# Kernel tuning notes

Hardware: AMD Instinct MI355X
Metric: run time of the kernel (lower is better)

## Reference

```python
import jax, jax.numpy as jnp
import numpy as np

B, C, H, W = 16, 512, 64, 64
K = 32


def setup_inputs() -> dict:
    key = jax.random.key(0)
    k1, k2, k3 = jax.random.split(key, 3)
    std = 1.0 / (64 * C) ** 0.5
    x = jax.random.normal(k1, (B, C, H, W), dtype=jnp.float32)
    codewords = jax.random.uniform(k2, (K, C), dtype=jnp.float32, minval=-std, maxval=std)
    scale = jax.random.uniform(k3, (K,), dtype=jnp.float32, minval=-1.0, maxval=0.0)
    return {"x": x, "codewords": codewords, "scale": scale}


def reference(x, codewords, scale):
    b, c, h, w = x.shape
    # (b, n, c) with n = h*w spatial positions
    xf = x.reshape(b, c, h * w).transpose(0, 2, 1)
    x2 = jnp.sum(xf * xf, axis=-1)                       # (b, n)
    c2 = jnp.sum(codewords * codewords, axis=-1)          # (k,)
    xc = jnp.einsum('bnc,kc->bnk', xf, codewords)         # (b, n, k)
    logits = scale[None, None, :] * (x2[:, :, None] - 2.0 * xc + c2[None, None, :])
    A = jax.nn.softmax(logits, axis=2)                    # (b, n, k)
    # sum_n A[b,n,k] * (x[b,n,c] - codewords[k,c])
    encoded = jnp.einsum('bnk,bnc->bkc', A, xf) - jnp.einsum('bnk,kc->bkc', A, codewords)
    return encoded
```

## Files before the change

kernel.cpp:

```cpp
#include <hip/hip_runtime.h>
#include <hip/hip_bf16.h>
#include <math.h>

#define BB 16
#define CC 512
#define NN 4096
#define KK 32

typedef __attribute__((ext_vector_type(8))) short short8;
typedef __attribute__((ext_vector_type(4))) float float4v;

static __device__ __forceinline__ unsigned short f2bf(float f) {
  unsigned u = __float_as_uint(f);
  u += 0x7FFF + ((u >> 16) & 1);
  return (unsigned short)(u >> 16);
}
static __device__ __forceinline__ float bf2f(unsigned short s) {
  return __uint_as_float(((unsigned)s) << 16);
}


__global__ __launch_bounds__(256) void prep_kernel(
    const float* __restrict__ cw, unsigned short* __restrict__ cwt2,
    float* __restrict__ c2, float* __restrict__ out) {
  int gid = blockIdx.x * 256 + threadIdx.x;
  float4v z = {0.f, 0.f, 0.f, 0.f};
  float4v* o4 = (float4v*)out;
#pragma unroll
  for (int j = 0; j < 4; ++j) o4[gid + j * 16384] = z;
  {
    int c = gid >> 5, k = gid & 31;
    cwt2[gid] = f2bf(cw[k * CC + c]);
  }
  __shared__ float c2p[KK][8];
  if (blockIdx.x == 0) {
    int k = threadIdx.x >> 3, j = threadIdx.x & 7;
    const float* row = cw + k * CC + j * 64;
    float s = 0.f;
    for (int i = 0; i < 64; ++i) s = fmaf(row[i], row[i], s);
    c2p[k][j] = s;
    __syncthreads();
    if (threadIdx.x < KK) {
      float t = 0.f;
      for (int j2 = 0; j2 < 8; ++j2) t += c2p[threadIdx.x][j2];
      c2[threadIdx.x] = t;
    }
  }
}

__global__ __launch_bounds__(256) void logits_kernel(
    const float* __restrict__ x, const unsigned short* __restrict__ cwt2,
    const float* __restrict__ c2g, const float* __restrict__ scale,
    unsigned short* __restrict__ A) {
  const int b = blockIdx.x >> 4;
  const int n0 = (blockIdx.x & 15) << 8;
  const int t = threadIdx.x;
  const int kq = t & 3;
  const int pq = t >> 2;

  __shared__ float Xl[2][8][258];
  __shared__ unsigned short Sm[256][34];

  const float* xb = x + (size_t)b * CC * NN + n0;

  float sc[8], cc2[8];
#pragma unroll
  for (int i = 0; i < 8; ++i) {
    sc[i] = scale[8 * kq + i];
    cc2[i] = c2g[8 * kq + i];
  }

  float acc[8][4];
#pragma unroll
  for (int i = 0; i < 8; ++i)
#pragma unroll
    for (int p = 0; p < 4; ++p) acc[i][p] = 0.f;
  float x2[4] = {0.f, 0.f, 0.f, 0.f};

  float4v pf[2];
#pragma unroll
  for (int j = 0; j < 2; ++j) {
    int f = t + 256 * j;
    int row = f >> 6, c4 = f & 63;
    pf[j] = *(const float4v*)(xb + (size_t)row * NN + c4 * 4);
  }
#pragma unroll
  for (int j = 0; j < 2; ++j) {
    int f = t + 256 * j;
    int row = f >> 6, c4 = f & 63;
    *(float4v*)&Xl[0][row][c4 * 4] = pf[j];
  }
  __syncthreads();

  int cur = 0;
  for (int ch = 0; ch < 64; ++ch) {
    const int cbase = ch * 8;
    if (ch < 63) {
#pragma unroll
      for (int j = 0; j < 2; ++j) {
        int f = t + 256 * j;
        int row = f >> 6, c4 = f & 63;
        pf[j] = *(const float4v*)(xb + (size_t)(cbase + 8 + row) * NN + c4 * 4);
      }
    }
#pragma unroll
    for (int c = 0; c < 8; ++c) {
      float4v xv = *(const float4v*)&Xl[cur][c][4 * pq];
      short8 cwv = *(const short8*)(cwt2 + (size_t)(cbase + c) * 32 + 8 * kq);
      float cf[8];
#pragma unroll
      for (int i = 0; i < 8; ++i) cf[i] = bf2f(((unsigned short*)&cwv)[i]);
      x2[0] = fmaf(xv.x, xv.x, x2[0]);
      x2[1] = fmaf(xv.y, xv.y, x2[1]);
      x2[2] = fmaf(xv.z, xv.z, x2[2]);
      x2[3] = fmaf(xv.w, xv.w, x2[3]);
#pragma unroll
      for (int i = 0; i < 8; ++i) {
        acc[i][0] = fmaf(cf[i], xv.x, acc[i][0]);
        acc[i][1] = fmaf(cf[i], xv.y, acc[i][1]);
        acc[i][2] = fmaf(cf[i], xv.z, acc[i][2]);
        acc[i][3] = fmaf(cf[i], xv.w, acc[i][3]);
      }
    }
    if (ch < 63) {
      int nxt = cur ^ 1;
#pragma unroll
      for (int j = 0; j < 2; ++j) {
        int f = t + 256 * j;
        int row = f >> 6, c4 = f & 63;
        *(float4v*)&Xl[nxt][row][c4 * 4] = pf[j];
      }
      __syncthreads();
      cur = nxt;
    }
  }

#pragma unroll
  for (int p = 0; p < 4; ++p) {
    float l[8];
    float m = -INFINITY;
#pragma unroll
    for (int i = 0; i < 8; ++i) {
      float lg = sc[i] * (x2[p] - 2.f * acc[i][p] + cc2[i]);
      l[i] = lg;
      m = fmaxf(m, lg);
    }
    m = fmaxf(m, __shfl_xor(m, 1));
    m = fmaxf(m, __shfl_xor(m, 2));
    float s = 0.f;
#pragma unroll
    for (int i = 0; i < 8; ++i) {
      float e = __expf(l[i] - m);
      l[i] = e;
      s += e;
    }
    s += __shfl_xor(s, 1);
    s += __shfl_xor(s, 2);
    float inv = 1.0f / s;
    const int pos = 4 * pq + p;
#pragma unroll
    for (int i = 0; i < 8; ++i) Sm[pos][8 * kq + i] = f2bf(l[i] * inv);
  }
  __syncthreads();

#pragma unroll
  for (int k = 0; k < KK; ++k) {
    A[((size_t)(b * KK + k)) * NN + n0 + t] = Sm[t][k];
  }
}

__global__ __launch_bounds__(256) void agg_kernel(
    const float* __restrict__ x, const unsigned short* __restrict__ A,
    float* __restrict__ out) {
  const int b = blockIdx.x >> 4;
  const int n0 = (blockIdx.x & 15) << 8;
  const int t = threadIdx.x;
  const int w = t >> 6;
  const int l = t & 63;
  const int l15 = l & 15;
  const int q = l >> 4;
  const int cw0 = 128 * w;

  float4v acc[8][2];
#pragma unroll
  for (int ct = 0; ct < 8; ++ct)
#pragma unroll
    for (int m = 0; m < 2; ++m) acc[ct][m] = (float4v){0.f, 0.f, 0.f, 0.f};

  const unsigned short* Ab = A + (size_t)b * KK * NN;
  const float* xb = x + (size_t)b * CC * NN;

  for (int s = 0; s < 8; ++s) {
    const int nb = n0 + s * 32 + q * 8;
    short8 a0 = *(const short8*)(Ab + (size_t)l15 * NN + nb);
    short8 a1 = *(const short8*)(Ab + (size_t)(16 + l15) * NN + nb);
#pragma unroll
    for (int ct = 0; ct < 8; ++ct) {
      const int c = cw0 + 16 * ct + l15;
      const float* xp = xb + (size_t)c * NN + nb;
      float4v x0 = *(const float4v*)xp;
      float4v x1 = *(const float4v*)(xp + 4);
      short8 bv;
      bv[0] = (short)f2bf(x0.x);
      bv[1] = (short)f2bf(x0.y);
      bv[2] = (short)f2bf(x0.z);
      bv[3] = (short)f2bf(x0.w);
      bv[4] = (short)f2bf(x1.x);
      bv[5] = (short)f2bf(x1.y);
      bv[6] = (short)f2bf(x1.z);
      bv[7] = (short)f2bf(x1.w);
      acc[ct][0] = __builtin_amdgcn_mfma_f32_16x16x32_bf16(a0, bv, acc[ct][0], 0, 0, 0);
      acc[ct][1] = __builtin_amdgcn_mfma_f32_16x16x32_bf16(a1, bv, acc[ct][1], 0, 0, 0);
    }
  }

#pragma unroll
  for (int ct = 0; ct < 8; ++ct) {
    const int c = cw0 + 16 * ct + l15;
#pragma unroll
    for (int m = 0; m < 2; ++m)
#pragma unroll
      for (int r = 0; r < 4; ++r) {
        int k = 16 * m + 4 * q + r;
        atomicAdd(&out[((size_t)(b * KK + k)) * CC + c], acc[ct][m][r]);
      }
  }
}

__global__ __launch_bounds__(256) void finalize_kernel(
    float* __restrict__ out, const unsigned short* __restrict__ A,
    const float* __restrict__ cw) {
  const int bk = blockIdx.x;
  const int k = bk & 31;
  const int t = threadIdx.x;
  const unsigned short* Ar = A + (size_t)bk * NN;

  float s = 0.f;
#pragma unroll
  for (int j = 0; j < 2; ++j) {
    short8 v = *(const short8*)(Ar + t * 16 + j * 8);
#pragma unroll
    for (int i = 0; i < 8; ++i) s += bf2f(((unsigned short*)&v)[i]);
  }
  s += __shfl_xor(s, 1);
  s += __shfl_xor(s, 2);
  s += __shfl_xor(s, 4);
  s += __shfl_xor(s, 8);
  s += __shfl_xor(s, 16);
  s += __shfl_xor(s, 32);

  __shared__ float red[4];
  __shared__ float asums;
  if ((t & 63) == 0) red[t >> 6] = s;
  __syncthreads();
  if (t == 0) asums = red[0] + red[1] + red[2] + red[3];
  __syncthreads();
  const float asum = asums;

#pragma unroll
  for (int j = 0; j < 2; ++j) {
    int c = t + 256 * j;
    out[(size_t)bk * CC + c] -= asum * cw[k * CC + c];
  }
}

extern "C" void kernel_launch(void* const* d_in, const int* in_sizes, int n_in,
                              void* d_out, int out_size, void* d_ws, size_t ws_size,
                              hipStream_t stream) {
  const float* x = (const float*)d_in[0];
  const float* cw = (const float*)d_in[1];
  const float* scale = (const float*)d_in[2];
  float* out = (float*)d_out;
  char* ws = (char*)d_ws;

  float* c2 = (float*)ws;
  unsigned short* cwt2 = (unsigned short*)(ws + 128);
  unsigned short* A = (unsigned short*)(ws + 32896);

  prep_kernel<<<64, 256, 0, stream>>>(cw, cwt2, c2, out);
  logits_kernel<<<256, 256, 0, stream>>>(x, cwt2, c2, scale, A);
  agg_kernel<<<256, 256, 0, stream>>>(x, A, out);
  finalize_kernel<<<512, 256, 0, stream>>>(out, A, cw);
}
```

Before: 275.3 us.

## Use MFMA for logits, fuse A row-sums into softmax, split agg by channels

The logits GEMM moves from scalar FP32 FMAs to bf16 MFMA. Each block stages a 64-position tile of x as bf16 in LDS and computes x^2 during staging. Per-(b,k) sums of A are now accumulated with atomics in the logits kernel, so the finalize kernel no longer rereads A and becomes a simple vectorised elementwise update. The aggregation kernel is split four ways over channels to launch 1024 blocks with higher occupancy, at the cost of more atomics and a reduction in bf16 precision for the logits dot product.

```diff
diff --git a/kernel.cpp b/kernel.cpp
--- a/kernel.cpp
+++ b/kernel.cpp
@@ -15,23 +15,18 @@
   u += 0x7FFF + ((u >> 16) & 1);
   return (unsigned short)(u >> 16);
 }
-static __device__ __forceinline__ float bf2f(unsigned short s) {
-  return __uint_as_float(((unsigned)s) << 16);
-}
 
 
 __global__ __launch_bounds__(256) void prep_kernel(
-    const float* __restrict__ cw, unsigned short* __restrict__ cwt2,
-    float* __restrict__ c2, float* __restrict__ out) {
+    const float* __restrict__ cw, unsigned short* __restrict__ cwB,
+    float* __restrict__ c2, float* __restrict__ asum, float* __restrict__ out) {
   int gid = blockIdx.x * 256 + threadIdx.x;
   float4v z = {0.f, 0.f, 0.f, 0.f};
   float4v* o4 = (float4v*)out;
 #pragma unroll
   for (int j = 0; j < 4; ++j) o4[gid + j * 16384] = z;
-  {
-    int c = gid >> 5, k = gid & 31;
-    cwt2[gid] = f2bf(cw[k * CC + c]);
-  }
+  if (gid < BB * KK) asum[gid] = 0.f;
+  cwB[gid] = f2bf(cw[gid]);
   __shared__ float c2p[KK][8];
   if (blockIdx.x == 0) {
     int k = threadIdx.x >> 3, j = threadIdx.x & 7;
@@ -48,142 +43,143 @@
   }
 }
 
-__global__ __launch_bounds__(256) void logits_kernel(
-    const float* __restrict__ x, const unsigned short* __restrict__ cwt2,
+__global__ __launch_bounds__(256, 2) void logits_kernel(
+    const float* __restrict__ x, const unsigned short* __restrict__ cwB,
     const float* __restrict__ c2g, const float* __restrict__ scale,
-    unsigned short* __restrict__ A) {
-  const int b = blockIdx.x >> 4;
-  const int n0 = (blockIdx.x & 15) << 8;
+    unsigned short* __restrict__ A, float* __restrict__ asum) {
+  const int b = blockIdx.x >> 6;
+  const int n0 = (blockIdx.x & 63) << 6;
   const int t = threadIdx.x;
-  const int kq = t & 3;
-  const int pq = t >> 2;
-
-  __shared__ float Xl[2][8][258];
-  __shared__ unsigned short Sm[256][34];
+
+  __shared__ unsigned short Xl[512][68];
+  __shared__ float Sx2p[16][68];
+  __shared__ float Sx2[64];
 
   const float* xb = x + (size_t)b * CC * NN + n0;
 
-  float sc[8], cc2[8];
-#pragma unroll
-  for (int i = 0; i < 8; ++i) {
-    sc[i] = scale[8 * kq + i];
-    cc2[i] = c2g[8 * kq + i];
-  }
-
-  float acc[8][4];
-#pragma unroll
-  for (int i = 0; i < 8; ++i)
-#pragma unroll
-    for (int p = 0; p < 4; ++p) acc[i][p] = 0.f;
-  float x2[4] = {0.f, 0.f, 0.f, 0.f};
-
-  float4v pf[2];
-#pragma unroll
-  for (int j = 0; j < 2; ++j) {
-    int f = t + 256 * j;
-    int row = f >> 6, c4 = f & 63;
-    pf[j] = *(const float4v*)(xb + (size_t)row * NN + c4 * 4);
-  }
-#pragma unroll
-  for (int j = 0; j < 2; ++j) {
-    int f = t + 256 * j;
-    int row = f >> 6, c4 = f & 63;
-    *(float4v*)&Xl[0][row][c4 * 4] = pf[j];
+  {
+    const int f4 = t & 15;
+    const int cr = t >> 4;
+    float x2p0 = 0.f, x2p1 = 0.f, x2p2 = 0.f, x2p3 = 0.f;
+    for (int cc = 0; cc < 512; cc += 64) {
+      float4v v[4];
+#pragma unroll
+      for (int i = 0; i < 4; ++i)
+        v[i] = *(const float4v*)(xb + (size_t)(cc + 16 * i + cr) * NN + 4 * f4);
+#pragma unroll
+      for (int i = 0; i < 4; ++i) {
+        x2p0 = fmaf(v[i].x, v[i].x, x2p0);
+        x2p1 = fmaf(v[i].y, v[i].y, x2p1);
+        x2p2 = fmaf(v[i].z, v[i].z, x2p2);
+        x2p3 = fmaf(v[i].w, v[i].w, x2p3);
+        unsigned short h0 = f2bf(v[i].x), h1 = f2bf(v[i].y);
+        unsigned short h2 = f2bf(v[i].z), h3 = f2bf(v[i].w);
+        unsigned p0 = (unsigned)h0 | ((unsigned)h1 << 16);
+        unsigned p1 = (unsigned)h2 | ((unsigned)h3 << 16);
+        uint2 pk = make_uint2(p0, p1);
+        *(uint2*)&Xl[cc + 16 * i + cr][4 * f4] = pk;
+      }
+    }
+    Sx2p[cr][4 * f4 + 0] = x2p0;
+    Sx2p[cr][4 * f4 + 1] = x2p1;
+    Sx2p[cr][4 * f4 + 2] = x2p2;
+    Sx2p[cr][4 * f4 + 3] = x2p3;
   }
   __syncthreads();
-
-  int cur = 0;
-  for (int ch = 0; ch < 64; ++ch) {
-    const int cbase = ch * 8;
-    if (ch < 63) {
-#pragma unroll
-      for (int j = 0; j < 2; ++j) {
-        int f = t + 256 * j;
-        int row = f >> 6, c4 = f & 63;
-        pf[j] = *(const float4v*)(xb + (size_t)(cbase + 8 + row) * NN + c4 * 4);
-      }
-    }
-#pragma unroll
-    for (int c = 0; c < 8; ++c) {
-      float4v xv = *(const float4v*)&Xl[cur][c][4 * pq];
-      short8 cwv = *(const short8*)(cwt2 + (size_t)(cbase + c) * 32 + 8 * kq);
-      float cf[8];
-#pragma unroll
-      for (int i = 0; i < 8; ++i) cf[i] = bf2f(((unsigned short*)&cwv)[i]);
-      x2[0] = fmaf(xv.x, xv.x, x2[0]);
-      x2[1] = fmaf(xv.y, xv.y, x2[1]);
-      x2[2] = fmaf(xv.z, xv.z, x2[2]);
-      x2[3] = fmaf(xv.w, xv.w, x2[3]);
-#pragma unroll
-      for (int i = 0; i < 8; ++i) {
-        acc[i][0] = fmaf(cf[i], xv.x, acc[i][0]);
-        acc[i][1] = fmaf(cf[i], xv.y, acc[i][1]);
-        acc[i][2] = fmaf(cf[i], xv.z, acc[i][2]);
-        acc[i][3] = fmaf(cf[i], xv.w, acc[i][3]);
-      }
-    }
-    if (ch < 63) {
-      int nxt = cur ^ 1;
-#pragma unroll
-      for (int j = 0; j < 2; ++j) {
-        int f = t + 256 * j;
-        int row = f >> 6, c4 = f & 63;
-        *(float4v*)&Xl[nxt][row][c4 * 4] = pf[j];
-      }
-      __syncthreads();
-      cur = nxt;
-    }
-  }
-
-#pragma unroll
-  for (int p = 0; p < 4; ++p) {
-    float l[8];
-    float m = -INFINITY;
-#pragma unroll
-    for (int i = 0; i < 8; ++i) {
-      float lg = sc[i] * (x2[p] - 2.f * acc[i][p] + cc2[i]);
-      l[i] = lg;
-      m = fmaxf(m, lg);
-    }
+  if (t < 64) {
+    float s = 0.f;
+#pragma unroll
+    for (int r = 0; r < 16; ++r) s += Sx2p[r][t];
+    Sx2[t] = s;
+  }
+  __syncthreads();
+
+  const int w = t >> 6;
+  const int l = t & 63;
+  const int l15 = l & 15;
+  const int q = l >> 4;
+  const int nrow = w * 16 + l15;
+
+  float4v acc0 = {0.f, 0.f, 0.f, 0.f};
+  float4v acc1 = {0.f, 0.f, 0.f, 0.f};
+
+  for (int cs = 0; cs < 512; cs += 32) {
+    const int cb = cs + q * 8;
+    short8 af;
+#pragma unroll
+    for (int j = 0; j < 8; ++j) af[j] = (short)Xl[cb + j][nrow];
+    short8 b0 = *(const short8*)(cwB + (size_t)l15 * CC + cb);
+    short8 b1 = *(const short8*)(cwB + (size_t)(16 + l15) * CC + cb);
+    acc0 = __builtin_amdgcn_mfma_f32_16x16x32_bf16(af, b0, acc0, 0, 0, 0);
+    acc1 = __builtin_amdgcn_mfma_f32_16x16x32_bf16(af, b1, acc1, 0, 0, 0);
+  }
+
+  const float sc0 = scale[l15], sc1 = scale[16 + l15];
+  const float cc0 = c2g[l15], cc1 = c2g[16 + l15];
+
+  float a0[4], a1[4];
+#pragma unroll
+  for (int r = 0; r < 4; ++r) {
+    const float xx = Sx2[w * 16 + 4 * q + r];
+    float l0 = sc0 * (xx - 2.f * acc0[r] + cc0);
+    float l1 = sc1 * (xx - 2.f * acc1[r] + cc1);
+    float m = fmaxf(l0, l1);
     m = fmaxf(m, __shfl_xor(m, 1));
     m = fmaxf(m, __shfl_xor(m, 2));
-    float s = 0.f;
-#pragma unroll
-    for (int i = 0; i < 8; ++i) {
-      float e = __expf(l[i] - m);
-      l[i] = e;
-      s += e;
-    }
+    m = fmaxf(m, __shfl_xor(m, 4));
+    m = fmaxf(m, __shfl_xor(m, 8));
+    float e0 = __expf(l0 - m), e1 = __expf(l1 - m);
+    float s = e0 + e1;
     s += __shfl_xor(s, 1);
     s += __shfl_xor(s, 2);
+    s += __shfl_xor(s, 4);
+    s += __shfl_xor(s, 8);
     float inv = 1.0f / s;
-    const int pos = 4 * pq + p;
-#pragma unroll
-    for (int i = 0; i < 8; ++i) Sm[pos][8 * kq + i] = f2bf(l[i] * inv);
-  }
-  __syncthreads();
-
-#pragma unroll
-  for (int k = 0; k < KK; ++k) {
-    A[((size_t)(b * KK + k)) * NN + n0 + t] = Sm[t][k];
-  }
-}
-
-__global__ __launch_bounds__(256) void agg_kernel(
+    a0[r] = e0 * inv;
+    a1[r] = e1 * inv;
+  }
+
+  {
+    unsigned p00 = (unsigned)f2bf(a0[0]) | ((unsigned)f2bf(a0[1]) << 16);
+    unsigned p01 = (unsigned)f2bf(a0[2]) | ((unsigned)f2bf(a0[3]) << 16);
+    unsigned p10 = (unsigned)f2bf(a1[0]) | ((unsigned)f2bf(a1[1]) << 16);
+    unsigned p11 = (unsigned)f2bf(a1[2]) | ((unsigned)f2bf(a1[3]) << 16);
+    unsigned short* A0 = A + ((size_t)(b * KK + l15)) * NN + n0 + w * 16 + 4 * q;
+    unsigned short* A1 = A + ((size_t)(b * KK + 16 + l15)) * NN + n0 + w * 16 + 4 * q;
+    *(uint2*)A0 = make_uint2(p00, p01);
+    *(uint2*)A1 = make_uint2(p10, p11);
+  }
+
+  {
+    float s0 = a0[0] + a0[1] + a0[2] + a0[3];
+    float s1 = a1[0] + a1[1] + a1[2] + a1[3];
+    s0 += __shfl_xor(s0, 16);
+    s0 += __shfl_xor(s0, 32);
+    s1 += __shfl_xor(s1, 16);
+    s1 += __shfl_xor(s1, 32);
+    if (q == 0) {
+      atomicAdd(&asum[b * KK + l15], s0);
+      atomicAdd(&asum[b * KK + 16 + l15], s1);
+    }
+  }
+}
+
+__global__ __launch_bounds__(256, 4) void agg_kernel(
     const float* __restrict__ x, const unsigned short* __restrict__ A,
     float* __restrict__ out) {
-  const int b = blockIdx.x >> 4;
+  const int b = blockIdx.x >> 6;
+  const int cg = (blockIdx.x >> 4) & 3;
   const int n0 = (blockIdx.x & 15) << 8;
   const int t = threadIdx.x;
   const int w = t >> 6;
   const int l = t & 63;
   const int l15 = l & 15;
   const int q = l >> 4;
-  const int cw0 = 128 * w;
-
-  float4v acc[8][2];
-#pragma unroll
-  for (int ct = 0; ct < 8; ++ct)
+  const int cw0 = cg * 128 + 32 * w;
+
+  float4v acc[2][2];
+#pragma unroll
+  for (int ct = 0; ct < 2; ++ct)
 #pragma unroll
     for (int m = 0; m < 2; ++m) acc[ct][m] = (float4v){0.f, 0.f, 0.f, 0.f};
 
@@ -195,7 +191,7 @@
     short8 a0 = *(const short8*)(Ab + (size_t)l15 * NN + nb);
     short8 a1 = *(const short8*)(Ab + (size_t)(16 + l15) * NN + nb);
 #pragma unroll
-    for (int ct = 0; ct < 8; ++ct) {
+    for (int ct = 0; ct < 2; ++ct) {
       const int c = cw0 + 16 * ct + l15;
       const float* xp = xb + (size_t)c * NN + nb;
       float4v x0 = *(const float4v*)xp;
@@ -215,7 +211,7 @@
   }
 
 #pragma unroll
-  for (int ct = 0; ct < 8; ++ct) {
+  for (int ct = 0; ct < 2; ++ct) {
     const int c = cw0 + 16 * ct + l15;
 #pragma unroll
     for (int m = 0; m < 2; ++m)
@@ -228,40 +224,20 @@
 }
 
 __global__ __launch_bounds__(256) void finalize_kernel(
-    float* __restrict__ out, const unsigned short* __restrict__ A,
+    float* __restrict__ out, const float* __restrict__ asum,
     const float* __restrict__ cw) {
-  const int bk = blockIdx.x;
-  const int k = bk & 31;
-  const int t = threadIdx.x;
-  const unsigned short* Ar = A + (size_t)bk * NN;
-
-  float s = 0.f;
-#pragma unroll
-  for (int j = 0; j < 2; ++j) {
-    short8 v = *(const short8*)(Ar + t * 16 + j * 8);
-#pragma unroll
-    for (int i = 0; i < 8; ++i) s += bf2f(((unsigned short*)&v)[i]);
-  }
-  s += __shfl_xor(s, 1);
-  s += __shfl_xor(s, 2);
-  s += __shfl_xor(s, 4);
-  s += __shfl_xor(s, 8);
-  s += __shfl_xor(s, 16);
-  s += __shfl_xor(s, 32);
-
-  __shared__ float red[4];
-  __shared__ float asums;
-  if ((t & 63) == 0) red[t >> 6] = s;
-  __syncthreads();
-  if (t == 0) asums = red[0] + red[1] + red[2] + red[3];
-  __syncthreads();
-  const float asum = asums;
-
-#pragma unroll
-  for (int j = 0; j < 2; ++j) {
-    int c = t + 256 * j;
-    out[(size_t)bk * CC + c] -= asum * cw[k * CC + c];
-  }
+  int idx = blockIdx.x * 256 + threadIdx.x;
+  int b = idx >> 12;
+  int k = (idx >> 7) & 31;
+  int c4 = idx & 127;
+  float4v o = ((float4v*)out)[idx];
+  float4v wv = ((const float4v*)cw)[k * 128 + c4];
+  float a = asum[b * KK + k];
+  o.x -= a * wv.x;
+  o.y -= a * wv.y;
+  o.z -= a * wv.z;
+  o.w -= a * wv.w;
+  ((float4v*)out)[idx] = o;
 }
 
 extern "C" void kernel_launch(void* const* d_in, const int* in_sizes, int n_in,
@@ -274,11 +250,12 @@
   char* ws = (char*)d_ws;
 
   float* c2 = (float*)ws;
-  unsigned short* cwt2 = (unsigned short*)(ws + 128);
-  unsigned short* A = (unsigned short*)(ws + 32896);
-
-  prep_kernel<<<64, 256, 0, stream>>>(cw, cwt2, c2, out);
-  logits_kernel<<<256, 256, 0, stream>>>(x, cwt2, c2, scale, A);
-  agg_kernel<<<256, 256, 0, stream>>>(x, A, out);
-  finalize_kernel<<<512, 256, 0, stream>>>(out, A, cw);
-}
+  unsigned short* cwB = (unsigned short*)(ws + 128);
+  float* asum = (float*)(ws + 32896);
+  unsigned short* A = (unsigned short*)(ws + 34944);
+
+  prep_kernel<<<64, 256, 0, stream>>>(cw, cwB, c2, asum, out);
+  logits_kernel<<<1024, 256, 0, stream>>>(x, cwB, c2, scale, A, asum);
+  agg_kernel<<<1024, 256, 0, stream>>>(x, A, out);
+  finalize_kernel<<<256, 256, 0, stream>>>(out, asum, cw);
+}
```

Measured after the change: 244.1 us. 1.13x faster.
